# Optimization experiments

Measured on AMD Instinct MI355X. Metric: run time of the kernel, lower is better.

Reference implementation:

```python
import jax, jax.numpy as jnp
import numpy as np

B, T, I, H, O = 4096, 200, 2, 64, 2


def setup_inputs() -> dict:
    key = jax.random.key(0)
    ks = jax.random.split(key, 7)
    s = 1.0 / np.sqrt(H)  # PyTorch LSTM init scale
    return {
        "x": jax.random.normal(ks[0], (B, T, I), dtype=jnp.float32),
        "W_ih": jax.random.uniform(ks[1], (4 * H, I), jnp.float32, -s, s),
        "W_hh": jax.random.uniform(ks[2], (4 * H, H), jnp.float32, -s, s),
        "b_ih": jax.random.uniform(ks[3], (4 * H,), jnp.float32, -s, s),
        "b_hh": jax.random.uniform(ks[4], (4 * H,), jnp.float32, -s, s),
        "W_fc": jax.random.uniform(ks[5], (O, H), jnp.float32, -s, s),
        "b_fc": jax.random.uniform(ks[6], (O,), jnp.float32, -s, s),
    }


def reference(x, W_ih, W_hh, b_ih, b_hh, W_fc, b_fc):
    # Precompute input-to-gate projections for all timesteps in one GEMM.
    # xg: [T, B, 4H] (time-major for scan)
    xg = jnp.einsum("bti,gi->tbg", x, W_ih) + (b_ih + b_hh)

    def step(carry, xt):
        h, c = carry  # [B, H] each
        gates = xt + h @ W_hh.T  # [B, 4H]
        i_g, f_g, g_g, o_g = jnp.split(gates, 4, axis=-1)  # PyTorch order: i, f, g, o
        i = jax.nn.sigmoid(i_g)
        f = jax.nn.sigmoid(f_g)
        g = jnp.tanh(g_g)
        o = jax.nn.sigmoid(o_g)
        c = f * c + i * g
        h = o * jnp.tanh(c)
        return (h, c), None

    h0 = jnp.zeros((x.shape[0], W_hh.shape[1]), dtype=x.dtype)
    c0 = jnp.zeros_like(h0)
    (h_last, _), _ = jax.lax.scan(step, (h0, c0), xg)
    return h_last @ W_fc.T + b_fc  # [B, O]
```

## Files before the change

### kernel.cpp

```cpp
#include <hip/hip_runtime.h>
#include <hip/hip_bf16.h>


#define B_ 4096
#define T_ 200

typedef _Float16 half8 __attribute__((ext_vector_type(8)));
typedef float f32x4 __attribute__((ext_vector_type(4)));

__device__ __forceinline__ float fsig(float x) {
    return __builtin_amdgcn_rcpf(1.0f + __builtin_amdgcn_exp2f(-1.4426950408889634f * x));
}
__device__ __forceinline__ float ftanh(float x) {
    return fmaf(-2.0f, __builtin_amdgcn_rcpf(1.0f + __builtin_amdgcn_exp2f(2.8853900817779268f * x)), 1.0f);
}

__global__ __launch_bounds__(1024) void lstm_kernel(
    const float* __restrict__ x,
    const float* __restrict__ W_ih,
    const float* __restrict__ W_hh,
    const float* __restrict__ b_ih,
    const float* __restrict__ b_hh,
    const float* __restrict__ W_fc,
    const float* __restrict__ b_fc,
    float* __restrict__ out)
{
    __shared__ float xs[16][404];
    __shared__ _Float16 h16[2][16][72];
    __shared__ float wfc[130];

    const int tid  = threadIdx.x;
    const int lane = tid & 63;
    const int w    = tid >> 6;
    const int wq   = w & 3;
    const int qr   = w >> 2;
    const int cidx = lane & 15;
    const int grp  = lane >> 4;
    const int r0   = blockIdx.x * 16;

    for (int i4 = tid; i4 < 1600; i4 += 1024) {
        const int row = i4 / 100;
        const int j4  = i4 - row * 100;
        reinterpret_cast<float4*>(&xs[row][0])[j4] =
            reinterpret_cast<const float4*>(x + (size_t)(r0 + row) * 400)[j4];
    }
    for (int i = tid; i < 1152; i += 1024)
        reinterpret_cast<unsigned int*>(&h16[0][0][0])[i] = 0u;
    if (tid < 130) wfc[tid] = (tid < 128) ? W_fc[tid] : b_fc[tid - 128];

    half8 bfrag[4][2];
    float wi0[4], wi1[4], bs[4];
    const int u = wq * 16 + cidx;
    #pragma unroll
    for (int m = 0; m < 4; ++m) {
        const int g = m * 64 + u;
        wi0[m] = W_ih[g * 2 + 0];
        wi1[m] = W_ih[g * 2 + 1];
        bs[m]  = b_ih[g] + b_hh[g];
        #pragma unroll
        for (int kt = 0; kt < 2; ++kt) {
            const float* p = W_hh + g * 64 + kt * 32 + grp * 8;
            const float4 lo = reinterpret_cast<const float4*>(p)[0];
            const float4 hi = reinterpret_cast<const float4*>(p)[1];
            half8 f;
            f[0] = (_Float16)lo.x; f[1] = (_Float16)lo.y;
            f[2] = (_Float16)lo.z; f[3] = (_Float16)lo.w;
            f[4] = (_Float16)hi.x; f[5] = (_Float16)hi.y;
            f[6] = (_Float16)hi.z; f[7] = (_Float16)hi.w;
            bfrag[m][kt] = f;
        }
    }

    const int arow = (cidx + qr) & 15;
    const int row  = (grp * 4 + qr) & 15;
    float cst = 0.f;

    __syncthreads();

    for (int t = 0; t < T_; ++t) {
        const int rd = t & 1;
        const _Float16* hb = &h16[rd][0][0];
        const half8 a0 = *reinterpret_cast<const half8*>(hb + arow * 72 + grp * 8);
        const half8 a1 = *reinterpret_cast<const half8*>(hb + arow * 72 + 32 + grp * 8);
        const float2 xv = *reinterpret_cast<const float2*>(&xs[row][2 * t]);

        float pre[4];
        #pragma unroll
        for (int m = 0; m < 4; ++m) {
            f32x4 a = {bs[m], bs[m], bs[m], bs[m]};
            a = __builtin_amdgcn_mfma_f32_16x16x32_f16(a0, bfrag[m][0], a, 0, 0, 0);
            a = __builtin_amdgcn_mfma_f32_16x16x32_f16(a1, bfrag[m][1], a, 0, 0, 0);
            pre[m] = fmaf(xv.y, wi1[m], fmaf(xv.x, wi0[m], a[0]));
        }

        const float ig = fsig(pre[0]);
        const float fg = fsig(pre[1]);
        const float gg = ftanh(pre[2]);
        const float og = fsig(pre[3]);
        cst = fmaf(fg, cst, ig * gg);
        const float hv = og * ftanh(cst);
        h16[rd ^ 1][row][u] = (_Float16)hv;
        __syncthreads();
    }

    if (tid < 32) {
        const int r = tid & 15;
        const int o = tid >> 4;
        float s = wfc[128 + o];
        #pragma unroll
        for (int k = 0; k < 64; ++k)
            s = fmaf(wfc[o * 64 + k], (float)h16[0][r][k], s);
        out[(size_t)(r0 + r) * 2 + o] = s;
    }
}

extern "C" void kernel_launch(void* const* d_in, const int* in_sizes, int n_in,
                              void* d_out, int out_size, void* d_ws, size_t ws_size,
                              hipStream_t stream) {
    const float* x    = (const float*)d_in[0];
    const float* W_ih = (const float*)d_in[1];
    const float* W_hh = (const float*)d_in[2];
    const float* b_ih = (const float*)d_in[3];
    const float* b_hh = (const float*)d_in[4];
    const float* W_fc = (const float*)d_in[5];
    const float* b_fc = (const float*)d_in[6];
    float* out = (float*)d_out;

    lstm_kernel<<<B_ / 16, 1024, 0, stream>>>(x, W_ih, W_hh, b_ih, b_hh, W_fc, b_fc, out);
}
```

Measured before the change: 115.5 us.

## Shrink blocks to 4 batch rows and fuse gate nonlinearities into shared reciprocals

Each block now handles 4 batch rows with 256 threads instead of 16 rows with 1024 threads, giving 1024 blocks and cheaper per-step barriers. The MFMA A operand broadcasts each of the 4 rows across 4 lanes, so much of the MFMA work is redundant. The gate weights are prescaled by log2(e) constants so exp2 can be applied directly, and the input projection is folded into the accumulator init. Sigmoid and tanh are merged algebraically so each step uses two reciprocals instead of five, with clamps added to avoid overflow.

```diff
diff --git a/kernel.cpp b/kernel.cpp
--- a/kernel.cpp
+++ b/kernel.cpp
@@ -8,14 +8,11 @@
 typedef _Float16 half8 __attribute__((ext_vector_type(8)));
 typedef float f32x4 __attribute__((ext_vector_type(4)));
 
-__device__ __forceinline__ float fsig(float x) {
-    return __builtin_amdgcn_rcpf(1.0f + __builtin_amdgcn_exp2f(-1.4426950408889634f * x));
-}
-__device__ __forceinline__ float ftanh(float x) {
-    return fmaf(-2.0f, __builtin_amdgcn_rcpf(1.0f + __builtin_amdgcn_exp2f(2.8853900817779268f * x)), 1.0f);
-}
+#define K1f 1.4426950408889634f
+#define K2f 2.8853900817779268f
+#define ECLAMP 40.0f
 
-__global__ __launch_bounds__(1024) void lstm_kernel(
+__global__ __launch_bounds__(256, 4) void lstm_kernel(
     const float* __restrict__ x,
     const float* __restrict__ W_ih,
     const float* __restrict__ W_hh,
@@ -25,87 +22,95 @@
     const float* __restrict__ b_fc,
     float* __restrict__ out)
 {
-    __shared__ float xs[16][404];
-    __shared__ _Float16 h16[2][16][72];
+    __shared__ float xs[4][404];
+    __shared__ _Float16 h16[2][4][76];
     __shared__ float wfc[130];
 
     const int tid  = threadIdx.x;
     const int lane = tid & 63;
     const int w    = tid >> 6;
-    const int wq   = w & 3;
-    const int qr   = w >> 2;
     const int cidx = lane & 15;
     const int grp  = lane >> 4;
-    const int r0   = blockIdx.x * 16;
+    const int r0   = blockIdx.x * 4;
 
-    for (int i4 = tid; i4 < 1600; i4 += 1024) {
+    for (int i4 = tid; i4 < 400; i4 += 256) {
         const int row = i4 / 100;
         const int j4  = i4 - row * 100;
         reinterpret_cast<float4*>(&xs[row][0])[j4] =
             reinterpret_cast<const float4*>(x + (size_t)(r0 + row) * 400)[j4];
     }
-    for (int i = tid; i < 1152; i += 1024)
+    for (int i = tid; i < 304; i += 256)
         reinterpret_cast<unsigned int*>(&h16[0][0][0])[i] = 0u;
     if (tid < 130) wfc[tid] = (tid < 128) ? W_fc[tid] : b_fc[tid - 128];
 
     half8 bfrag[4][2];
     float wi0[4], wi1[4], bs[4];
-    const int u = wq * 16 + cidx;
+    const int u = w * 16 + cidx;
     #pragma unroll
     for (int m = 0; m < 4; ++m) {
+        const float sc = (m == 2) ? K2f : -K1f;
         const int g = m * 64 + u;
-        wi0[m] = W_ih[g * 2 + 0];
-        wi1[m] = W_ih[g * 2 + 1];
-        bs[m]  = b_ih[g] + b_hh[g];
+        wi0[m] = W_ih[g * 2 + 0] * sc;
+        wi1[m] = W_ih[g * 2 + 1] * sc;
+        bs[m]  = (b_ih[g] + b_hh[g]) * sc;
         #pragma unroll
         for (int kt = 0; kt < 2; ++kt) {
             const float* p = W_hh + g * 64 + kt * 32 + grp * 8;
             const float4 lo = reinterpret_cast<const float4*>(p)[0];
             const float4 hi = reinterpret_cast<const float4*>(p)[1];
             half8 f;
-            f[0] = (_Float16)lo.x; f[1] = (_Float16)lo.y;
-            f[2] = (_Float16)lo.z; f[3] = (_Float16)lo.w;
-            f[4] = (_Float16)hi.x; f[5] = (_Float16)hi.y;
-            f[6] = (_Float16)hi.z; f[7] = (_Float16)hi.w;
+            f[0] = (_Float16)(lo.x * sc); f[1] = (_Float16)(lo.y * sc);
+            f[2] = (_Float16)(lo.z * sc); f[3] = (_Float16)(lo.w * sc);
+            f[4] = (_Float16)(hi.x * sc); f[5] = (_Float16)(hi.y * sc);
+            f[6] = (_Float16)(hi.z * sc); f[7] = (_Float16)(hi.w * sc);
             bfrag[m][kt] = f;
         }
     }
 
-    const int arow = (cidx + qr) & 15;
-    const int row  = (grp * 4 + qr) & 15;
+    const int arow = cidx >> 2;
+    const int row  = grp;
     float cst = 0.f;
 
     __syncthreads();
 
     for (int t = 0; t < T_; ++t) {
         const int rd = t & 1;
+        const float2 xv = *reinterpret_cast<const float2*>(&xs[row][2 * t]);
         const _Float16* hb = &h16[rd][0][0];
-        const half8 a0 = *reinterpret_cast<const half8*>(hb + arow * 72 + grp * 8);
-        const half8 a1 = *reinterpret_cast<const half8*>(hb + arow * 72 + 32 + grp * 8);
-        const float2 xv = *reinterpret_cast<const float2*>(&xs[row][2 * t]);
+        const half8 a0 = *reinterpret_cast<const half8*>(hb + arow * 76 + grp * 8);
+        const half8 a1 = *reinterpret_cast<const half8*>(hb + arow * 76 + 32 + grp * 8);
 
         float pre[4];
         #pragma unroll
         for (int m = 0; m < 4; ++m) {
-            f32x4 a = {bs[m], bs[m], bs[m], bs[m]};
+            const float proj = fmaf(xv.y, wi1[m], fmaf(xv.x, wi0[m], bs[m]));
+            f32x4 a = {proj, proj, proj, proj};
             a = __builtin_amdgcn_mfma_f32_16x16x32_f16(a0, bfrag[m][0], a, 0, 0, 0);
             a = __builtin_amdgcn_mfma_f32_16x16x32_f16(a1, bfrag[m][1], a, 0, 0, 0);
-            pre[m] = fmaf(xv.y, wi1[m], fmaf(xv.x, wi0[m], a[0]));
+            pre[m] = a[0];
         }
 
-        const float ig = fsig(pre[0]);
-        const float fg = fsig(pre[1]);
-        const float gg = ftanh(pre[2]);
-        const float og = fsig(pre[3]);
-        cst = fmaf(fg, cst, ig * gg);
-        const float hv = og * ftanh(cst);
+        const float Ei = __builtin_amdgcn_exp2f(fminf(pre[0], ECLAMP));
+        const float Ef = __builtin_amdgcn_exp2f(fminf(pre[1], ECLAMP));
+        const float Eg = __builtin_amdgcn_exp2f(fminf(pre[2], ECLAMP));
+        const float Eo = __builtin_amdgcn_exp2f(fminf(pre[3], ECLAMP));
+
+        const float fEf = 1.0f + Ef;
+        const float P   = (1.0f + Ei) * (Eg + 1.0f);
+        const float r1  = __builtin_amdgcn_rcpf(P * fEf);
+        cst = fmaf(cst, P, (Eg - 1.0f) * fEf) * r1;
+
+        const float Ec = __builtin_amdgcn_exp2f(fminf(K2f * cst, ECLAMP));
+        const float r2 = __builtin_amdgcn_rcpf((1.0f + Eo) * (Ec + 1.0f));
+        const float hv = (Ec - 1.0f) * r2;
+
         h16[rd ^ 1][row][u] = (_Float16)hv;
         __syncthreads();
     }
 
-    if (tid < 32) {
-        const int r = tid & 15;
-        const int o = tid >> 4;
+    if (tid < 8) {
+        const int r = tid & 3;
+        const int o = tid >> 2;
         float s = wfc[128 + o];
         #pragma unroll
         for (int k = 0; k < 64; ++k)
@@ -126,5 +131,5 @@
     const float* b_fc = (const float*)d_in[6];
     float* out = (float*)d_out;
 
-    lstm_kernel<<<B_ / 16, 1024, 0, stream>>>(x, W_ih, W_hh, b_ih, b_hh, W_fc, b_fc, out);
+    lstm_kernel<<<B_ / 4, 256, 0, stream>>>(x, W_ih, W_hh, b_ih, b_hh, W_fc, b_fc, out);
 }
```

After: 203.9 us. 76.5% more time.
